# Optimization experiments

Measured on AMD Instinct MI355X. Metric: run time of the kernel, lower is better.

## Reference

```python
import jax, jax.numpy as jnp
import numpy as np

NUM_CODES = 8192
CODE_DIM = 64
DECAY = 0.99
EPS = 1e-05


def setup_inputs() -> dict:
    key = jax.random.key(0)
    k1, k2 = jax.random.split(key)
    z = jax.random.normal(k1, (8, CODE_DIM, 64, 64), dtype=jnp.float32)
    embed = jax.random.normal(k2, (NUM_CODES, CODE_DIM), dtype=jnp.float32)
    embed = embed / jnp.linalg.norm(embed, axis=1, keepdims=True)  # F.normalize(dim=1)
    cluster_size = jnp.zeros((NUM_CODES,), dtype=jnp.float32)
    embed_avg = embed * 1.0
    return {"z": z, "embed": embed, "cluster_size": cluster_size, "embed_avg": embed_avg}


def reference(z, embed, cluster_size, embed_avg):
    B, C, H, W = z.shape
    # (B,C,H,W) -> (N, C), N = B*H*W
    flat = jnp.transpose(z, (0, 2, 3, 1)).reshape(-1, C)
    x2 = jnp.sum(flat * flat, axis=1, keepdims=True)
    e2 = jnp.sum(embed * embed, axis=1)[None, :]
    logits = x2 + e2 - 2.0 * (flat @ embed.T)
    codes = jnp.argmin(logits, axis=1)
    # gather nearest code vectors, restore (B,C,H,W)
    z_q = jnp.transpose(embed[codes].reshape(B, H, W, C), (0, 3, 1, 2))
    # EMA update (training path; equivalent to one-hot matmul via segment sums)
    cs_batch = jax.ops.segment_sum(jnp.ones_like(codes, dtype=flat.dtype), codes, num_segments=NUM_CODES)
    embed_sum = jax.ops.segment_sum(flat, codes, num_segments=NUM_CODES)
    new_cluster_size = cluster_size * DECAY + cs_batch * (1.0 - DECAY)
    new_embed_avg = embed_avg * DECAY + embed_sum * (1.0 - DECAY)
    n = jnp.sum(new_cluster_size)
    cs_smoothed = (new_cluster_size + EPS) / (n + NUM_CODES * EPS) * n
    new_embed = new_embed_avg / cs_smoothed[:, None]
    new_embed = new_embed / jnp.linalg.norm(new_embed, axis=1, keepdims=True)
    return z_q, codes.reshape(B, H, W), new_embed, new_cluster_size, new_embed_avg
```

## Files before the change

### kernel.cpp

```cpp
#include <hip/hip_runtime.h>
#include <math.h>
#include <float.h>

#define NPTS   32768
#define NCODES 8192
#define D      64
#define HWSZ   4096
#define KSPLIT 8
#define NSTAGE 8

#define DECAY_F 0.99f
#define OMD_F   ((float)(1.0 - 0.99))
#define EPS_F   1e-5f

typedef __attribute__((ext_vector_type(8)))  short bf16x8;
typedef __attribute__((ext_vector_type(8)))  unsigned short us8;
typedef __attribute__((ext_vector_type(4)))  float f32x4;
typedef __attribute__((ext_vector_type(16))) float f32x16;

#define ZQ_OFF    0
#define CODES_OFF 2097152
#define NE_OFF    2129920
#define NCS_OFF   2654208
#define NEA_OFF   2662400

#define WS_PSUM   0
#define WS_ME2    64
#define WS_HIST   8256
#define WS_BOFF   16448
#define WS_BOFF2  24640
#define WS_CODES  32832
#define WS_ORDER  65600
#define WS_PMG    98368
#define WS_EB     1146944
#define WS_ZROW   1671232

__device__ __forceinline__ unsigned short f2bf(float x) {
    unsigned int u = __float_as_uint(x);
    unsigned int r = (u + 0x7fffu + ((u >> 16) & 1u)) >> 16;
    return (unsigned short)r;
}
__device__ __forceinline__ float bf2f(unsigned short b) {
    return __uint_as_float(((unsigned int)b) << 16);
}

__global__ __launch_bounds__(256) void k_prep_e(
    const float* __restrict__ embed, const float* __restrict__ cs_in,
    unsigned short* __restrict__ eb0, unsigned short* __restrict__ eb1,
    float* __restrict__ me2, int* __restrict__ hist, float* __restrict__ psum)
{
    __shared__ float wsum[4];
    const int tid = threadIdx.x;
    int c = blockIdx.x * 256 + tid;
    const float4* src = (const float4*)(embed + (size_t)c * D);
    float row[64];
    float s2 = 0.f;
#pragma unroll
    for (int i = 0; i < 16; ++i) {
        float4 v = src[i];
        row[i * 4 + 0] = v.x; row[i * 4 + 1] = v.y;
        row[i * 4 + 2] = v.z; row[i * 4 + 3] = v.w;
        s2 += v.x * v.x; s2 += v.y * v.y; s2 += v.z * v.z; s2 += v.w * v.w;
    }
    size_t base = (size_t)(c >> 7) * 8192 + (size_t)(c & 127) * 8;
#pragma unroll
    for (int s = 0; s < 8; ++s) {
        us8 v0, v1;
#pragma unroll
        for (int j = 0; j < 8; ++j) {
            float x = row[s * 8 + j];
            unsigned short a = f2bf(x);
            float r1 = x - bf2f(a);
            v0[j] = a; v1[j] = f2bf(r1);
        }
        *(us8*)(eb0 + base + (size_t)s * 1024) = v0;
        *(us8*)(eb1 + base + (size_t)s * 1024) = v1;
    }
    me2[c] = -0.5f * s2;
    hist[c] = 0;
    float t = cs_in[c];
    t += __shfl_xor(t, 32); t += __shfl_xor(t, 16); t += __shfl_xor(t, 8);
    t += __shfl_xor(t, 4);  t += __shfl_xor(t, 2);  t += __shfl_xor(t, 1);
    if ((tid & 63) == 0) wsum[tid >> 6] = t;
    __syncthreads();
    if (tid == 0) psum[blockIdx.x] = (wsum[0] + wsum[1]) + (wsum[2] + wsum[3]);
}

#define MFMA32 __builtin_amdgcn_mfma_f32_32x32x16_bf16

#define TOP2(nt, g, gi) { \
    bool c1 = (g) > b1m[nt]; \
    bool c2 = (g) > b2m[nt]; \
    b2m[nt] = c1 ? b1m[nt] : (c2 ? (g) : b2m[nt]); \
    b2g[nt] = c1 ? b1g[nt] : (c2 ? (gi) : b2g[nt]); \
    b1m[nt] = c1 ? (g) : b1m[nt]; \
    b1g[nt] = c1 ? (gi) : b1g[nt]; }

__global__ __launch_bounds__(256, 2) void k_argmin_mfma(
    const float* __restrict__ z,
    const unsigned short* __restrict__ eb0, const unsigned short* __restrict__ eb1,
    const float* __restrict__ me2g,
    float* __restrict__ pmg)
{
    __shared__ unsigned short ets[2 * 8192];
    __shared__ float me2s[128];

    const int tid = threadIdx.x;
    const int l = tid & 63;
    const int w = tid >> 6;
    const int l31 = l & 31;
    const int hi = l >> 5;
    const int split = blockIdx.x >> 6;
    const int pgrp  = blockIdx.x & 63;
    const int n0    = pgrp * 512;
    const int b     = n0 >> 12;
    const int hw0   = n0 & 4095;
    const int ptw   = n0 + w * 128;

    const float* zb = z + (size_t)b * D * HWSZ;
    us8 zf[4][2][4];
#pragma unroll
    for (int nt = 0; nt < 4; ++nt) {
        const int hwp = hw0 + w * 128 + nt * 32 + l31;
#pragma unroll
        for (int kc = 0; kc < 4; ++kc) {
            us8 p0, p1;
#pragma unroll
            for (int j = 0; j < 8; ++j) {
                float x = zb[(size_t)(kc * 16 + hi * 8 + j) * HWSZ + hwp];
                unsigned short a = f2bf(x);
                float r = x - bf2f(a);
                p0[j] = a; p1[j] = f2bf(r);
            }
            zf[nt][0][kc] = p0; zf[nt][1][kc] = p1;
        }
    }

    float b1m[4], b2m[4]; int b1g[4], b2g[4];
#pragma unroll
    for (int nt = 0; nt < 4; ++nt) {
        b1m[nt] = -FLT_MAX; b2m[nt] = -FLT_MAX; b1g[nt] = 0; b2g[nt] = 0;
    }

    for (int stg = 0; stg < NSTAGE; ++stg) {
        const int sg = split * NSTAGE + stg;
        __syncthreads();
        {
            const char* s0 = (const char*)eb0 + (size_t)sg * 16384;
            const char* s1 = (const char*)eb1 + (size_t)sg * 16384;
            float4 tmp[8];
#pragma unroll
            for (int i = 0; i < 8; ++i) {
                int flat = i * 256 + tid;
                const char* sp = (flat < 1024) ? s0 : s1;
                tmp[i] = *(const float4*)(sp + (size_t)(flat & 1023) * 16);
            }
#pragma unroll
            for (int i = 0; i < 8; ++i) {
                int flat = i * 256 + tid;
                *(float4*)((char*)ets + (size_t)flat * 16) = tmp[i];
            }
            if (tid < 128) me2s[tid] = me2g[sg * 128 + tid];
        }
        __syncthreads();

#pragma unroll
        for (int ct = 0; ct < 4; ++ct) {
            f32x4 meq[4];
#pragma unroll
            for (int q = 0; q < 4; ++q)
                meq[q] = *(const f32x4*)(me2s + ct * 32 + q * 8 + hi * 4);

            f32x16 acc[4];
#pragma unroll
            for (int nt = 0; nt < 4; ++nt)
#pragma unroll
                for (int q = 0; q < 4; ++q)
#pragma unroll
                    for (int r = 0; r < 4; ++r)
                        acc[nt][q * 4 + r] = meq[q][r];

#pragma unroll
            for (int kc = 0; kc < 4; ++kc) {
                bf16x8 ea0 = *(const bf16x8*)((const char*)ets
                              + (size_t)(kc * 2 + hi) * 2048 + (size_t)(ct * 32 + l31) * 16);
                bf16x8 ea1 = *(const bf16x8*)((const char*)ets + 16384
                              + (size_t)(kc * 2 + hi) * 2048 + (size_t)(ct * 32 + l31) * 16);
#pragma unroll
                for (int nt = 0; nt < 4; ++nt)
                    acc[nt] = MFMA32(ea1, (bf16x8)zf[nt][0][kc], acc[nt], 0, 0, 0);
#pragma unroll
                for (int nt = 0; nt < 4; ++nt)
                    acc[nt] = MFMA32(ea0, (bf16x8)zf[nt][1][kc], acc[nt], 0, 0, 0);
#pragma unroll
                for (int nt = 0; nt < 4; ++nt)
                    acc[nt] = MFMA32(ea0, (bf16x8)zf[nt][0][kc], acc[nt], 0, 0, 0);
            }

            const int gib = sg * 32 + ct * 8 + hi;
#pragma unroll
            for (int nt = 0; nt < 4; ++nt) {
#pragma unroll
                for (int q = 0; q < 4; ++q) {
                    float g = fmaxf(fmaxf(acc[nt][4 * q + 0], acc[nt][4 * q + 1]),
                                    fmaxf(acc[nt][4 * q + 2], acc[nt][4 * q + 3]));
                    TOP2(nt, g, gib + q * 2)
                }
            }
        }
    }

#pragma unroll
    for (int nt = 0; nt < 4; ++nt) {
        float o1 = __shfl_xor(b1m[nt], 32); int o1g = __shfl_xor(b1g[nt], 32);
        float o2 = __shfl_xor(b2m[nt], 32); int o2g = __shfl_xor(b2g[nt], 32);
        float n1m, n2m; int n1g, n2g;
        if (o1 > b1m[nt]) {
            n1m = o1; n1g = o1g;
            if (b1m[nt] >= o2) { n2m = b1m[nt]; n2g = b1g[nt]; } else { n2m = o2; n2g = o2g; }
        } else {
            n1m = b1m[nt]; n1g = b1g[nt];
            if (o1 >= b2m[nt]) { n2m = o1; n2g = o1g; } else { n2m = b2m[nt]; n2g = b2g[nt]; }
        }
        b1m[nt] = n1m; b1g[nt] = n1g; b2m[nt] = n2m; b2g[nt] = n2g;
    }
    if (l < 32) {
#pragma unroll
        for (int nt = 0; nt < 4; ++nt) {
            int pt = ptw + nt * 32 + l31;
            float4 v = {b1m[nt], __int_as_float(b1g[nt]), b2m[nt], __int_as_float(b2g[nt])};
            *(float4*)(pmg + (size_t)pt * 32 + split * 4) = v;
        }
    }
}

__global__ __launch_bounds__(256) void k_refine(
    const float* __restrict__ z, const float* __restrict__ embed,
    const float* __restrict__ me2, const float* __restrict__ pmg,
    int* __restrict__ codes_i, float* __restrict__ out_codes,
    float* __restrict__ zq, int* __restrict__ hist, float* __restrict__ zrow)
{
    __shared__ float  xs[64 * 32];
    __shared__ float4 smg[256];
    __shared__ float  sbm[256];
    __shared__ int    sbi[256];
    const int tid = threadIdx.x;
    const int pi = tid & 31, s = tid >> 5;
    const int n0 = blockIdx.x * 32;
    const int b = n0 >> 12, hw0 = n0 & 4095;
    const int n = n0 + pi;

    {
        float4 v = *((const float4*)pmg + (size_t)n0 * 8 + tid);
        smg[(tid & 7) * 32 + (tid >> 3)] = v;
    }
    const float* zb = z + (size_t)b * D * HWSZ + hw0;
#pragma unroll
    for (int i = 0; i < 8; ++i) {
        int c = s * 8 + i;
        xs[c * 32 + pi] = zb[(size_t)c * HWSZ + pi];
    }
    __syncthreads();
    float x[64];
#pragma unroll
    for (int c = 0; c < 64; ++c) x[c] = xs[c * 32 + pi];

    float t1 = -FLT_MAX, t2 = -FLT_MAX; int g1 = 0, g2 = 0;
#pragma unroll
    for (int j = 0; j < 8; ++j) {
        float4 v = smg[j * 32 + pi];
        float m1 = v.x; int a1 = __float_as_int(v.y);
        float m2 = v.z; int a2 = __float_as_int(v.w);
        if (m1 > t1) { t2 = t1; g2 = g1; t1 = m1; g1 = a1; }
        else if (m1 > t2) { t2 = m1; g2 = a1; }
        if (m2 > t1) { t2 = t1; g2 = g1; t1 = m2; g1 = a2; }
        else if (m2 > t2) { t2 = m2; g2 = a2; }
    }

    const int ci = ((s < 4) ? g1 : g2) * 4 + (s & 3);
    const float4* er = (const float4*)(embed + (size_t)ci * D);
    float d0 = 0.f, d1 = 0.f, d2 = 0.f, d3 = 0.f;
#pragma unroll
    for (int q = 0; q < 16; ++q) {
        float4 e4 = er[q];
        d0 = fmaf(x[4 * q + 0], e4.x, d0);
        d1 = fmaf(x[4 * q + 1], e4.y, d1);
        d2 = fmaf(x[4 * q + 2], e4.z, d2);
        d3 = fmaf(x[4 * q + 3], e4.w, d3);
    }
    float m = ((d0 + d1) + (d2 + d3)) + me2[ci];
    sbm[tid] = m; sbi[tid] = ci;
    __syncthreads();

    if (s == 0) {
        float B = sbm[pi]; int I = sbi[pi];
#pragma unroll
        for (int t = 1; t < 8; ++t) {
            float mm = sbm[t * 32 + pi]; int ii = sbi[t * 32 + pi];
            if (mm > B || (mm == B && ii < I)) { B = mm; I = ii; }
        }
        codes_i[n] = I;
        out_codes[n] = (float)I;
        atomicAdd(&hist[I], 1);
        const float* err = embed + (size_t)I * D;
        size_t zoff = (size_t)b * D * HWSZ + hw0 + pi;
#pragma unroll 8
        for (int c = 0; c < 64; ++c) zq[zoff + (size_t)c * HWSZ] = err[c];
    }
    {
        float4 a4 = {x[s * 8 + 0], x[s * 8 + 1], x[s * 8 + 2], x[s * 8 + 3]};
        float4 b4 = {x[s * 8 + 4], x[s * 8 + 5], x[s * 8 + 6], x[s * 8 + 7]};
        *(float4*)(zrow + (size_t)n * 64 + s * 8) = a4;
        *(float4*)(zrow + (size_t)n * 64 + s * 8 + 4) = b4;
    }
}

__global__ __launch_bounds__(1024) void k_scan(
    const int* __restrict__ hist, int* __restrict__ binoff, int* __restrict__ binoff2)
{
    __shared__ int wtot[16];
    __shared__ int wbase[16];
    const int tid = threadIdx.x;
    const int lane = tid & 63, w = tid >> 6;
    int v[8]; int s = 0;
#pragma unroll
    for (int i = 0; i < 8; ++i) { v[i] = hist[tid * 8 + i]; s += v[i]; }
    int inc = s;
#pragma unroll
    for (int off = 1; off < 64; off <<= 1) {
        int t = __shfl_up(inc, off);
        if (lane >= off) inc += t;
    }
    if (lane == 63) wtot[w] = inc;
    __syncthreads();
    if (tid == 0) {
        int a = 0;
#pragma unroll
        for (int i = 0; i < 16; ++i) { int t = wtot[i]; wbase[i] = a; a += t; }
    }
    __syncthreads();
    int excl = wbase[w] + (inc - s);
#pragma unroll
    for (int i = 0; i < 8; ++i) {
        binoff[tid * 8 + i] = excl;
        binoff2[tid * 8 + i] = excl;
        excl += v[i];
    }
}

__global__ void k_reorder(const int* __restrict__ codes_i,
                          int* __restrict__ binoff2, int* __restrict__ order)
{
    int n = blockIdx.x * 256 + threadIdx.x;
    int c = codes_i[n];
    int r = atomicAdd(&binoff2[c], 1);
    order[r] = n;
}

__global__ __launch_bounds__(256) void k_accum(
    const int* __restrict__ hist, const int* __restrict__ binoff,
    const int* __restrict__ order, const float* __restrict__ zrow,
    const float* __restrict__ cs, const float* __restrict__ eavg,
    const float* __restrict__ psum,
    float* __restrict__ out_ncs, float* __restrict__ out_nea, float* __restrict__ out_ne)
{
    int k = blockIdx.x * 4 + (threadIdx.x >> 6);
    int lane = threadIdx.x & 63;
    int cnt = hist[k], base = binoff[k];
    float acc = 0.f;
    for (int i = 0; i < cnt; ++i) {
        int p = order[base + i];
        acc += zrow[(size_t)p * 64 + lane];
    }
    float S = 0.f;
#pragma unroll
    for (int i = 0; i < 32; ++i) S += psum[i];
    float n = DECAY_F * S + OMD_F * (float)NPTS;

    float v = cs[k] * DECAY_F + (float)cnt * OMD_F;
    if (lane == 0) out_ncs[k] = v;

    int idx = k * D + lane;
    float ea = eavg[idx] * DECAY_F + acc * OMD_F;
    out_nea[idx] = ea;
    float csm = (v + EPS_F) / (n + (float)NCODES * EPS_F) * n;
    float u = ea / csm;
    float ss = u * u;
    ss += __shfl_xor(ss, 32);
    ss += __shfl_xor(ss, 16);
    ss += __shfl_xor(ss, 8);
    ss += __shfl_xor(ss, 4);
    ss += __shfl_xor(ss, 2);
    ss += __shfl_xor(ss, 1);
    out_ne[idx] = u / sqrtf(ss);
}

extern "C" void kernel_launch(void* const* d_in, const int* in_sizes, int n_in,
                              void* d_out, int out_size, void* d_ws, size_t ws_size,
                              hipStream_t stream) {
    const float* z     = (const float*)d_in[0];
    const float* embed = (const float*)d_in[1];
    const float* cs    = (const float*)d_in[2];
    const float* eavg  = (const float*)d_in[3];

    float* out = (float*)d_out;
    float* zq        = out + ZQ_OFF;
    float* out_codes = out + CODES_OFF;
    float* out_ne    = out + NE_OFF;
    float* out_ncs   = out + NCS_OFF;
    float* out_nea   = out + NEA_OFF;

    float* ws = (float*)d_ws;
    float* psum   = ws + WS_PSUM;
    float* me2    = ws + WS_ME2;
    int*   hist   = (int*)(ws + WS_HIST);
    int*   boff   = (int*)(ws + WS_BOFF);
    int*   boff2  = (int*)(ws + WS_BOFF2);
    int*   codesi = (int*)(ws + WS_CODES);
    int*   order  = (int*)(ws + WS_ORDER);
    float* pmg    = ws + WS_PMG;
    float* zrow   = ws + WS_ZROW;
    unsigned short* eb0 = (unsigned short*)(ws + WS_EB);
    unsigned short* eb1 = (unsigned short*)(ws + WS_EB + 262144);

    k_prep_e<<<NCODES / 256, 256, 0, stream>>>(embed, cs, eb0, eb1, me2, hist, psum);
    k_argmin_mfma<<<64 * KSPLIT, 256, 0, stream>>>(z, eb0, eb1, me2, pmg);
    k_refine<<<NPTS / 32, 256, 0, stream>>>(z, embed, me2, pmg,
                                            codesi, out_codes, zq, hist, zrow);
    k_scan<<<1, 1024, 0, stream>>>(hist, boff, boff2);
    k_reorder<<<NPTS / 256, 256, 0, stream>>>(codesi, boff2, order);
    k_accum<<<NCODES / 4, 256, 0, stream>>>(hist, boff, order, zrow, cs, eavg, psum,
                                            out_ncs, out_nea, out_ne);
}
```

Before: 137.7 us.

## Read codebook fragments directly from global, halve points per block, coarsen candidate groups

The argmin kernel stops staging the bf16 codebook tiles in shared memory and instead loads each MFMA operand straight from global memory (L2/L1 cached), removing the per-stage barriers and LDS copy. Each block now handles 256 points instead of 512 with occupancy hint raised to 4 blocks/CU, and the grid doubles. Candidate groups are coarsened from 4 to 8 codes per max, so the refine kernel now evaluates 8 codes per thread-slot pair across two candidate groups using a remapping function. This trades LDS traffic and syncs for more redundant global/L1 loads and more refine FMA work.

```diff
diff --git a/kernel.cpp b/kernel.cpp
--- a/kernel.cpp
+++ b/kernel.cpp
@@ -96,32 +96,39 @@
     b1m[nt] = c1 ? (g) : b1m[nt]; \
     b1g[nt] = c1 ? (gi) : b1g[nt]; }
 
-__global__ __launch_bounds__(256, 2) void k_argmin_mfma(
+#define GMAX8(a, o) fmaxf(fmaxf(fmaxf(a[o+0], a[o+1]), fmaxf(a[o+2], a[o+3])), \
+                          fmaxf(fmaxf(a[o+4], a[o+5]), fmaxf(a[o+6], a[o+7])))
+
+__global__ __launch_bounds__(256, 4) void k_argmin_mfma(
     const float* __restrict__ z,
     const unsigned short* __restrict__ eb0, const unsigned short* __restrict__ eb1,
     const float* __restrict__ me2g,
     float* __restrict__ pmg)
 {
-    __shared__ unsigned short ets[2 * 8192];
-    __shared__ float me2s[128];
+    __shared__ float me2s[1024];
 
     const int tid = threadIdx.x;
     const int l = tid & 63;
     const int w = tid >> 6;
     const int l31 = l & 31;
     const int hi = l >> 5;
-    const int split = blockIdx.x >> 6;
-    const int pgrp  = blockIdx.x & 63;
-    const int n0    = pgrp * 512;
+    const int split = blockIdx.x >> 7;
+    const int pgrp  = blockIdx.x & 127;
+    const int n0    = pgrp * 256;
     const int b     = n0 >> 12;
     const int hw0   = n0 & 4095;
-    const int ptw   = n0 + w * 128;
+    const int ptw   = n0 + w * 64;
+
+    {
+        f32x4 v = *(const f32x4*)(me2g + split * 1024 + tid * 4);
+        *(f32x4*)(me2s + tid * 4) = v;
+    }
 
     const float* zb = z + (size_t)b * D * HWSZ;
-    us8 zf[4][2][4];
-#pragma unroll
-    for (int nt = 0; nt < 4; ++nt) {
-        const int hwp = hw0 + w * 128 + nt * 32 + l31;
+    us8 zf[2][2][4];
+#pragma unroll
+    for (int nt = 0; nt < 2; ++nt) {
+        const int hwp = hw0 + w * 64 + nt * 32 + l31;
 #pragma unroll
         for (int kc = 0; kc < 4; ++kc) {
             us8 p0, p1;
@@ -135,83 +142,59 @@
             zf[nt][0][kc] = p0; zf[nt][1][kc] = p1;
         }
     }
-
-    float b1m[4], b2m[4]; int b1g[4], b2g[4];
-#pragma unroll
-    for (int nt = 0; nt < 4; ++nt) {
-        b1m[nt] = -FLT_MAX; b2m[nt] = -FLT_MAX; b1g[nt] = 0; b2g[nt] = 0;
-    }
-
+    __syncthreads();
+
+    float b1m[2] = {-FLT_MAX, -FLT_MAX}, b2m[2] = {-FLT_MAX, -FLT_MAX};
+    int   b1g[2] = {0, 0},               b2g[2] = {0, 0};
+
+    const int eoff = (size_t)0 + (l31 * 16);
     for (int stg = 0; stg < NSTAGE; ++stg) {
         const int sg = split * NSTAGE + stg;
-        __syncthreads();
-        {
-            const char* s0 = (const char*)eb0 + (size_t)sg * 16384;
-            const char* s1 = (const char*)eb1 + (size_t)sg * 16384;
-            float4 tmp[8];
-#pragma unroll
-            for (int i = 0; i < 8; ++i) {
-                int flat = i * 256 + tid;
-                const char* sp = (flat < 1024) ? s0 : s1;
-                tmp[i] = *(const float4*)(sp + (size_t)(flat & 1023) * 16);
-            }
-#pragma unroll
-            for (int i = 0; i < 8; ++i) {
-                int flat = i * 256 + tid;
-                *(float4*)((char*)ets + (size_t)flat * 16) = tmp[i];
-            }
-            if (tid < 128) me2s[tid] = me2g[sg * 128 + tid];
-        }
-        __syncthreads();
+        const char* e0t = (const char*)eb0 + (size_t)sg * 16384;
+        const char* e1t = (const char*)eb1 + (size_t)sg * 16384;
 
 #pragma unroll
         for (int ct = 0; ct < 4; ++ct) {
-            f32x4 meq[4];
-#pragma unroll
-            for (int q = 0; q < 4; ++q)
-                meq[q] = *(const f32x4*)(me2s + ct * 32 + q * 8 + hi * 4);
-
-            f32x16 acc[4];
-#pragma unroll
-            for (int nt = 0; nt < 4; ++nt)
-#pragma unroll
-                for (int q = 0; q < 4; ++q)
-#pragma unroll
-                    for (int r = 0; r < 4; ++r)
-                        acc[nt][q * 4 + r] = meq[q][r];
-
-#pragma unroll
-            for (int kc = 0; kc < 4; ++kc) {
-                bf16x8 ea0 = *(const bf16x8*)((const char*)ets
-                              + (size_t)(kc * 2 + hi) * 2048 + (size_t)(ct * 32 + l31) * 16);
-                bf16x8 ea1 = *(const bf16x8*)((const char*)ets + 16384
-                              + (size_t)(kc * 2 + hi) * 2048 + (size_t)(ct * 32 + l31) * 16);
-#pragma unroll
-                for (int nt = 0; nt < 4; ++nt)
-                    acc[nt] = MFMA32(ea1, (bf16x8)zf[nt][0][kc], acc[nt], 0, 0, 0);
-#pragma unroll
-                for (int nt = 0; nt < 4; ++nt)
-                    acc[nt] = MFMA32(ea0, (bf16x8)zf[nt][1][kc], acc[nt], 0, 0, 0);
-#pragma unroll
-                for (int nt = 0; nt < 4; ++nt)
-                    acc[nt] = MFMA32(ea0, (bf16x8)zf[nt][0][kc], acc[nt], 0, 0, 0);
-            }
-
-            const int gib = sg * 32 + ct * 8 + hi;
-#pragma unroll
-            for (int nt = 0; nt < 4; ++nt) {
-#pragma unroll
-                for (int q = 0; q < 4; ++q) {
-                    float g = fmaxf(fmaxf(acc[nt][4 * q + 0], acc[nt][4 * q + 1]),
-                                    fmaxf(acc[nt][4 * q + 2], acc[nt][4 * q + 3]));
-                    TOP2(nt, g, gib + q * 2)
+            f32x16 acc0, acc1;
+#pragma unroll
+            for (int q = 0; q < 4; ++q) {
+                f32x4 mq = *(const f32x4*)(me2s + stg * 128 + ct * 32 + q * 8 + hi * 4);
+#pragma unroll
+                for (int r = 0; r < 4; ++r) {
+                    acc0[q * 4 + r] = mq[r];
+                    acc1[q * 4 + r] = mq[r];
                 }
             }
-        }
-    }
-
-#pragma unroll
-    for (int nt = 0; nt < 4; ++nt) {
+
+#pragma unroll
+            for (int kc = 0; kc < 4; ++kc) {
+                const size_t off = (size_t)(kc * 2 + hi) * 2048 + (size_t)(ct * 32 + l31) * 16;
+                bf16x8 ea0 = *(const bf16x8*)(e0t + off);
+                bf16x8 ea1 = *(const bf16x8*)(e1t + off);
+                acc0 = MFMA32(ea1, (bf16x8)zf[0][0][kc], acc0, 0, 0, 0);
+                acc1 = MFMA32(ea1, (bf16x8)zf[1][0][kc], acc1, 0, 0, 0);
+                acc0 = MFMA32(ea0, (bf16x8)zf[0][1][kc], acc0, 0, 0, 0);
+                acc1 = MFMA32(ea0, (bf16x8)zf[1][1][kc], acc1, 0, 0, 0);
+                acc0 = MFMA32(ea0, (bf16x8)zf[0][0][kc], acc0, 0, 0, 0);
+                acc1 = MFMA32(ea0, (bf16x8)zf[1][0][kc], acc1, 0, 0, 0);
+            }
+
+            const int gb = sg * 16 + ct * 4 + hi;
+            {
+                float g00 = GMAX8(acc0, 0);
+                float g01 = GMAX8(acc0, 8);
+                float g10 = GMAX8(acc1, 0);
+                float g11 = GMAX8(acc1, 8);
+                TOP2(0, g00, gb)
+                TOP2(0, g01, gb + 2)
+                TOP2(1, g10, gb)
+                TOP2(1, g11, gb + 2)
+            }
+        }
+    }
+
+#pragma unroll
+    for (int nt = 0; nt < 2; ++nt) {
         float o1 = __shfl_xor(b1m[nt], 32); int o1g = __shfl_xor(b1g[nt], 32);
         float o2 = __shfl_xor(b2m[nt], 32); int o2g = __shfl_xor(b2g[nt], 32);
         float n1m, n2m; int n1g, n2g;
@@ -226,12 +209,17 @@
     }
     if (l < 32) {
 #pragma unroll
-        for (int nt = 0; nt < 4; ++nt) {
+        for (int nt = 0; nt < 2; ++nt) {
             int pt = ptw + nt * 32 + l31;
             float4 v = {b1m[nt], __int_as_float(b1g[nt]), b2m[nt], __int_as_float(b2g[nt])};
             *(float4*)(pmg + (size_t)pt * 32 + split * 4) = v;
         }
     }
+}
+
+__device__ __forceinline__ int grp_code(int g, int s) {
+    int base = (g >> 4) * 128 + ((g >> 2) & 3) * 32 + ((g >> 1) & 1) * 16 + (g & 1) * 4;
+    return base + (s & 3) + ((s >> 2) & 1) * 8;
 }
 
 __global__ __launch_bounds__(256) void k_refine(
@@ -277,19 +265,24 @@
         else if (m2 > t2) { t2 = m2; g2 = a2; }
     }
 
-    const int ci = ((s < 4) ? g1 : g2) * 4 + (s & 3);
-    const float4* er = (const float4*)(embed + (size_t)ci * D);
-    float d0 = 0.f, d1 = 0.f, d2 = 0.f, d3 = 0.f;
-#pragma unroll
-    for (int q = 0; q < 16; ++q) {
-        float4 e4 = er[q];
-        d0 = fmaf(x[4 * q + 0], e4.x, d0);
-        d1 = fmaf(x[4 * q + 1], e4.y, d1);
-        d2 = fmaf(x[4 * q + 2], e4.z, d2);
-        d3 = fmaf(x[4 * q + 3], e4.w, d3);
-    }
-    float m = ((d0 + d1) + (d2 + d3)) + me2[ci];
-    sbm[tid] = m; sbi[tid] = ci;
+    float bm = -FLT_MAX; int bi = 0x7fffffff;
+#pragma unroll
+    for (int cset = 0; cset < 2; ++cset) {
+        const int ci = grp_code(cset ? g2 : g1, s);
+        const float4* er = (const float4*)(embed + (size_t)ci * D);
+        float d0 = 0.f, d1 = 0.f, d2 = 0.f, d3 = 0.f;
+#pragma unroll
+        for (int q = 0; q < 16; ++q) {
+            float4 e4 = er[q];
+            d0 = fmaf(x[4 * q + 0], e4.x, d0);
+            d1 = fmaf(x[4 * q + 1], e4.y, d1);
+            d2 = fmaf(x[4 * q + 2], e4.z, d2);
+            d3 = fmaf(x[4 * q + 3], e4.w, d3);
+        }
+        float m = ((d0 + d1) + (d2 + d3)) + me2[ci];
+        if (m > bm || (m == bm && ci < bi)) { bm = m; bi = ci; }
+    }
+    sbm[tid] = bm; sbi[tid] = bi;
     __syncthreads();
 
     if (s == 0) {
@@ -424,7 +417,7 @@
     unsigned short* eb1 = (unsigned short*)(ws + WS_EB + 262144);
 
     k_prep_e<<<NCODES / 256, 256, 0, stream>>>(embed, cs, eb0, eb1, me2, hist, psum);
-    k_argmin_mfma<<<64 * KSPLIT, 256, 0, stream>>>(z, eb0, eb1, me2, pmg);
+    k_argmin_mfma<<<128 * KSPLIT, 256, 0, stream>>>(z, eb0, eb1, me2, pmg);
     k_refine<<<NPTS / 32, 256, 0, stream>>>(z, embed, me2, pmg,
                                             codesi, out_codes, zq, hist, zrow);
     k_scan<<<1, 1024, 0, stream>>>(hist, boff, boff2);
```

New measurement: 206.7 us. 50.1% more time.
